# Kernel tuning notes

Measured on AMD Instinct MI355X. Metric: run time of the kernel, lower is better.

Reference implementation:

```python
import jax, jax.numpy as jnp
import numpy as np

K = 9          # neighbors per node (loop=False)
BN_EPS = 1e-5  # BatchNorm2d eps


def setup_inputs() -> dict:
    key = jax.random.key(0)
    k1, k2, k3 = jax.random.split(key, 3)
    B, C, H, W_ = 16, 384, 32, 32
    x = jax.random.normal(k1, (B, C, H, W_), dtype=jnp.float32)
    # GCNConv linear weight (PyG stores [out, in]; y = x @ W.T) and bias
    Wg = jax.random.normal(k2, (C, C), dtype=jnp.float32) / np.sqrt(C)
    bg = jax.random.normal(k3, (C,), dtype=jnp.float32) * 0.02
    gamma = jnp.ones((C,), dtype=jnp.float32)
    beta = jnp.zeros((C,), dtype=jnp.float32)
    return {"x": x, "Wg": Wg, "bg": bg, "gamma": gamma, "beta": beta}


def _knn_indices(xn):
    # xn: [B, N, C] -> neighbor indices [B, N, K] (self excluded)
    sq = jnp.sum(xn * xn, axis=-1)                       # [B, N]
    d = sq[:, :, None] + sq[:, None, :] - 2.0 * jnp.einsum("bnc,bmc->bnm", xn, xn)
    N = xn.shape[1]
    d = d + jnp.eye(N, dtype=xn.dtype) * jnp.finfo(xn.dtype).max  # exclude self
    _, nbr = jax.lax.top_k(-d, K)                        # [B, N, K]
    return nbr


def reference(x, Wg, bg, gamma, beta):
    B, C, H, W_ = x.shape
    N = H * W_
    BN_nodes = B * N
    shortcut = x

    # Flatten to nodes: [B*N, C]
    xn = jnp.transpose(x, (0, 2, 3, 1)).reshape(B, N, C)

    # Per-graph kNN in feature space (PyG knn_graph, flow source_to_target:
    # edges from neighbor (src) to query node (dst))
    nbr = _knn_indices(xn)                                # [B, N, K]
    offs = (jnp.arange(B) * N)[:, None, None]             # [B,1,1]
    src = (nbr + offs).reshape(-1)                        # [B*N*K]
    dst = jnp.broadcast_to(jnp.arange(N)[None, :, None] + offs, (B, N, K)).reshape(-1)

    # GCNConv: add self loops, symmetric normalization
    loops = jnp.arange(BN_nodes)
    src = jnp.concatenate([src, loops])
    dst = jnp.concatenate([dst, loops])

    xw = xn.reshape(BN_nodes, C) @ Wg.T                   # node-wise linear

    deg = jax.ops.segment_sum(jnp.ones_like(dst, dtype=xw.dtype), dst, num_segments=BN_nodes)
    dinv = jax.lax.rsqrt(deg)                             # deg >= 1 due to self loops
    norm = dinv[src] * dinv[dst]                          # [E]

    out = jax.ops.segment_sum(norm[:, None] * xw[src], dst, num_segments=BN_nodes) + bg

    # Back to B x C x H x W
    out = jnp.transpose(out.reshape(B, H, W_, C), (0, 3, 1, 2))

    # BatchNorm2d (training-mode batch statistics, biased variance)
    mu = jnp.mean(out, axis=(0, 2, 3), keepdims=True)
    var = jnp.mean((out - mu) ** 2, axis=(0, 2, 3), keepdims=True)
    out = gamma[None, :, None, None] * (out - mu) * jax.lax.rsqrt(var + BN_EPS) + beta[None, :, None, None]

    # GELU + residual (drop_path = 0 -> identity)
    out = jax.nn.gelu(out) + shortcut
    return out
```

## Files before the change

### kernel.cpp

```cpp
#include <hip/hip_runtime.h>
#include <math.h>

#define B_ 16
#define C_ 384
#define N_ 1024
#define K_ 9

typedef _Float16 f16x8 __attribute__((ext_vector_type(8)));
typedef _Float16 f16x4 __attribute__((ext_vector_type(4)));
typedef float f32x4 __attribute__((ext_vector_type(4)));
typedef unsigned long long u64;

__device__ __forceinline__ void gld_lds16(const void* g, void* l) {
  __builtin_amdgcn_global_load_lds((const __attribute__((address_space(1))) void*)g,
                                   (__attribute__((address_space(3))) void*)l, 16, 0, 0);
}

__global__ void k_cvt(const float* __restrict__ x, ushort* __restrict__ xhT,
                      ushort* __restrict__ xlT) {
  const int bid = blockIdx.x;
  const int ct = bid % 12;
  const int nt = (bid / 12) & 15;
  const int b = bid / 192;
  const int c0 = ct * 32, n0 = nt * 64;
  __shared__ float ld[32 * 65];
  const int t = threadIdx.x;
  {
    const int c = t >> 3, n8 = (t & 7) * 8;
    const float* src = x + ((size_t)(b * C_ + c0 + c) * N_ + n0 + n8);
    float4 v0 = *(const float4*)src;
    float4 v1 = *(const float4*)(src + 4);
    float vv[8] = {v0.x, v0.y, v0.z, v0.w, v1.x, v1.y, v1.z, v1.w};
#pragma unroll
    for (int j = 0; j < 8; ++j) ld[c * 65 + n8 + j] = vv[j];
  }
  __syncthreads();
  {
    const int n = t >> 2, c8 = (t & 3) * 8;
    f16x8 hv, lv;
#pragma unroll
    for (int j = 0; j < 8; ++j) {
      float v = ld[(c8 + j) * 65 + n];
      _Float16 h = (_Float16)v;
      _Float16 l = (_Float16)(v - (float)h);
      hv[j] = h;
      lv[j] = l;
    }
    const size_t off = (size_t)(b * N_ + n0 + n) * C_ + c0 + c8;
    *(f16x8*)(xhT + off) = hv;
    *(f16x8*)(xlT + off) = lv;
  }
}

__global__ void k_cvtw(const float* __restrict__ Wg, ushort* __restrict__ WgH,
                       ushort* __restrict__ WgL) {
  const int i = (blockIdx.x * 256 + threadIdx.x) * 4;
  float4 v = *(const float4*)(Wg + i);
  float vv[4] = {v.x, v.y, v.z, v.w};
  f16x4 hv, lv;
#pragma unroll
  for (int j = 0; j < 4; ++j) {
    _Float16 h = (_Float16)vv[j];
    hv[j] = h;
    lv[j] = (_Float16)(vv[j] - (float)h);
  }
  *(f16x4*)(WgH + i) = hv;
  *(f16x4*)(WgL + i) = lv;
}

__global__ void k_sq(const float* __restrict__ x, float* __restrict__ sq) {
  const int idx = blockIdx.x * blockDim.x + threadIdx.x;
  const int b = idx >> 10, n = idx & 1023;
  const float* xb = x + (size_t)b * C_ * N_ + n;
  double s = 0.0;
#pragma unroll 4
  for (int c = 0; c < C_; ++c) {
    float v = xb[(size_t)c * N_];
    s = fma((double)v, (double)v, s);
  }
  sq[idx] = (float)s;
}

__global__ __launch_bounds__(256, 2) void k_gram(const ushort* __restrict__ xhT,
                                                 const ushort* __restrict__ xlT,
                                                 const float* __restrict__ sq,
                                                 float* __restrict__ D, int base_b, int nb) {
  const int bid = blockIdx.x;
  int b_local, pid;
  if (nb >= 8) {
    const int x = bid & 7, j = bid >> 3, grp = nb >> 3;
    b_local = x * grp + (j >> 6);
    pid = j & 63;
  } else {
    b_local = bid >> 6;
    pid = bid & 63;
  }
  const int b = base_b + b_local;
  const int rt = pid >> 3, mt = pid & 7;
  const int n0 = rt * 128, m0 = mt * 128;

  __shared__ alignas(16) char sm[2][32768];
  const int t = threadIdx.x;
  const int lane = t & 63, wid = t >> 6, quad = lane >> 4, lrow = lane & 15;
  const int wr = wid >> 1, wc = wid & 1;
  const int lrow4 = lane >> 2, lpos = lane & 3;

  const char* src = (const char*)((wid & 1) ? xlT : xhT) +
                    (size_t)(b * N_ + ((wid >> 1) ? m0 : n0)) * C_ * 2;

  f32x4 acc[4][4];
#pragma unroll
  for (int mi = 0; mi < 4; ++mi)
#pragma unroll
    for (int ni = 0; ni < 4; ++ni) acc[mi][ni] = (f32x4){0.f, 0.f, 0.f, 0.f};

  auto stage = [&](int it) {
    char* dst = sm[it & 1] + wid * 8192;
    const int ktB = it * 64;
#pragma unroll
    for (int i = 0; i < 8; ++i) {
      const int row = i * 16 + lrow4;
      const int swz = lpos ^ ((row >> 1) & 3);
      gld_lds16(src + (size_t)row * 768 + ktB + swz * 16, dst + i * 1024 + lane * 16);
    }
  };

  stage(0);
  for (int it = 0; it < 12; ++it) {
    __syncthreads();
    if (it < 11) stage(it + 1);
    const char* smb = sm[it & 1];
    f16x8 ah[4], al[4];
#pragma unroll
    for (int mi = 0; mi < 4; ++mi) {
      const int row = wr * 64 + mi * 16 + lrow;
      const int off = row * 64 + (quad ^ ((row >> 1) & 3)) * 16;
      ah[mi] = *(const f16x8*)(smb + off);
      al[mi] = *(const f16x8*)(smb + 8192 + off);
    }
#pragma unroll
    for (int ni = 0; ni < 4; ++ni) {
      const int row = wc * 64 + ni * 16 + lrow;
      const int off = row * 64 + (quad ^ ((row >> 1) & 3)) * 16;
      f16x8 bh = *(const f16x8*)(smb + 16384 + off);
      f16x8 bl = *(const f16x8*)(smb + 24576 + off);
#pragma unroll
      for (int mi = 0; mi < 4; ++mi) {
        acc[mi][ni] = __builtin_amdgcn_mfma_f32_16x16x32_f16(ah[mi], bh, acc[mi][ni], 0, 0, 0);
        acc[mi][ni] = __builtin_amdgcn_mfma_f32_16x16x32_f16(al[mi], bh, acc[mi][ni], 0, 0, 0);
        acc[mi][ni] = __builtin_amdgcn_mfma_f32_16x16x32_f16(ah[mi], bl, acc[mi][ni], 0, 0, 0);
      }
    }
  }

  const float* sqb = sq + b * N_;
  float sqm[4];
#pragma unroll
  for (int ni = 0; ni < 4; ++ni) sqm[ni] = sqb[m0 + wc * 64 + ni * 16 + lrow];
  float sqn_[4][4];
#pragma unroll
  for (int mi = 0; mi < 4; ++mi)
#pragma unroll
    for (int r = 0; r < 4; ++r) sqn_[mi][r] = sqb[n0 + wr * 64 + mi * 16 + quad * 4 + r];

  float* Db = D + (size_t)b_local * N_ * N_;
#pragma unroll
  for (int mi = 0; mi < 4; ++mi)
#pragma unroll
    for (int ni = 0; ni < 4; ++ni)
#pragma unroll
      for (int r = 0; r < 4; ++r) {
        const int ng = n0 + wr * 64 + mi * 16 + quad * 4 + r;
        const int mg = m0 + wc * 64 + ni * 16 + lrow;
        float d = fmaf(-2.f, acc[mi][ni][r], sqn_[mi][r] + sqm[ni]);
        if (ng == mg) d = 3.402823466e38f;
        Db[(size_t)ng * N_ + mg] = d;
      }
}

__device__ __forceinline__ void ce2f(float& a, float& b) {
  float lo = fminf(a, b), hi = fmaxf(a, b);
  a = lo;
  b = hi;
}

__global__ __launch_bounds__(256) void k_scan(const float* __restrict__ D,
                                              int* __restrict__ nbr, int base_node) {
  const int t = threadIdx.x;
  const int lane = t & 63, wid = t >> 6;
  const int g = lane >> 5;
  const int ll = lane & 31;
  const int nl = blockIdx.x * 8 + wid * 2 + g;
  const float* row = D + (size_t)nl * N_ + ll * 32;
  float v[32];
#pragma unroll
  for (int i = 0; i < 8; ++i) {
    float4 q = *(const float4*)(row + i * 4);
    v[i * 4 + 0] = q.x;
    v[i * 4 + 1] = q.y;
    v[i * 4 + 2] = q.z;
    v[i * 4 + 3] = q.w;
  }
  float key[9];
#pragma unroll
  for (int k = 0; k < 9; ++k) key[k] = 3.402823466e38f;
#pragma unroll
  for (int j = 0; j < 32; ++j) {
    key[8] = fminf(key[8], v[j]);
#pragma unroll
    for (int s = 8; s >= 1; --s) ce2f(key[s - 1], key[s]);
  }
#pragma unroll
  for (int lvl = 1; lvl < 32; lvl <<= 1) {
    float pk[9];
#pragma unroll
    for (int k = 0; k < 9; ++k) pk[k] = __shfl_xor(key[k], lvl, 64);
    float m[9];
#pragma unroll
    for (int k = 0; k < 9; ++k) m[k] = fminf(key[k], pk[8 - k]);
    ce2f(m[0], m[8]);
    ce2f(m[1], m[5]); ce2f(m[2], m[6]); ce2f(m[3], m[7]); ce2f(m[4], m[8]);
    ce2f(m[1], m[3]); ce2f(m[2], m[4]); ce2f(m[5], m[7]); ce2f(m[6], m[8]);
    ce2f(m[1], m[2]); ce2f(m[3], m[4]); ce2f(m[5], m[6]); ce2f(m[7], m[8]);
#pragma unroll
    for (int k = 0; k < 9; ++k) key[k] = m[k];
  }
  const float v9 = key[8];
  int c_lt = 0;
#pragma unroll
  for (int k = 0; k < 8; ++k) c_lt += (key[k] < v9) ? 1 : 0;

  unsigned lt_mask = 0u, eq_mask = 0u;
#pragma unroll
  for (int j = 0; j < 32; ++j) {
    lt_mask |= (v[j] < v9) ? (1u << j) : 0u;
    eq_mask |= (v[j] == v9) ? (1u << j) : 0u;
  }
  const int lt_cnt = __popc(lt_mask), eq_cnt = __popc(eq_mask);
  int packed = lt_cnt | (eq_cnt << 16);
  int run = packed;
#pragma unroll
  for (int off = 1; off < 32; off <<= 1) {
    int q = __shfl_up(run, off, 32);
    if (ll >= off) run += q;
  }
  const int pref = run - packed;
  const int lt_pref = pref & 0xFFFF, eq_pref = pref >> 16;

  int* np = nbr + (size_t)(base_node + nl) * K_;
  int slot = lt_pref;
  unsigned m = lt_mask;
  while (m) {
    int j = __builtin_ctz(m);
    m &= m - 1;
    np[slot++] = ll * 32 + j;
  }
  slot = c_lt + eq_pref;
  m = eq_mask;
  while (m && slot < 9) {
    int j = __builtin_ctz(m);
    m &= m - 1;
    np[slot++] = ll * 32 + j;
  }
}

__global__ __launch_bounds__(256, 3) void k_xw(const ushort* __restrict__ xhT,
                                               const ushort* __restrict__ xlT,
                                               const ushort* __restrict__ WgH,
                                               const ushort* __restrict__ WgL,
                                               float* __restrict__ xw) {
  const int bid = blockIdx.x;
  const int xcd = bid & 7, j = bid >> 3;
  const int pair = xcd * 16 + j / 6;
  const int ct = j % 6;
  const int b = pair >> 3, nt = pair & 7;
  const int co0 = ct * 64, n0 = nt * 128;
  __shared__ alignas(16) char sm[2][24576];
  const int t = threadIdx.x;
  const int lane = t & 63, wid = t >> 6, quad = lane >> 4, lrow = lane & 15;
  const int wr = wid >> 1, wc = wid & 1;
  const int lrow4 = lane >> 2, lpos = lane & 3;

  f32x4 acc[2][4];
#pragma unroll
  for (int mi = 0; mi < 2; ++mi)
#pragma unroll
    for (int ni = 0; ni < 4; ++ni) acc[mi][ni] = (f32x4){0.f, 0.f, 0.f, 0.f};

  const char* asrc[2] = {(const char*)(WgH + (size_t)co0 * C_),
                         (const char*)(WgL + (size_t)co0 * C_)};
  const char* bsrc[2] = {(const char*)(xhT + (size_t)(b * N_ + n0) * C_),
                         (const char*)(xlT + (size_t)(b * N_ + n0) * C_)};

  auto stage = [&](int it) {
    char* dst = sm[it & 1];
    const int ktB = it * 64;
#pragma unroll
    for (int i = 0; i < 6; ++i) {
      const int c = wid * 6 + i;
      const char* src;
      int base, row;
      if (c < 8) {
        const int arr = c >> 2, sub = c & 3;
        src = asrc[arr];
        base = arr * 4096 + sub * 1024;
        row = sub * 16 + lrow4;
      } else {
        const int cc = c - 8, arr = cc >> 3, sub = cc & 7;
        src = bsrc[arr];
        base = 8192 + arr * 8192 + sub * 1024;
        row = sub * 16 + lrow4;
      }
      const int swz = lpos ^ ((row >> 1) & 3);
      gld_lds16(src + (size_t)row * 768 + ktB + swz * 16, dst + base + lane * 16);
    }
  };

  stage(0);
  for (int it = 0; it < 12; ++it) {
    __syncthreads();
    if (it < 11) stage(it + 1);
    const char* smb = sm[it & 1];
    f16x8 bh[4], bl[4];
#pragma unroll
    for (int ni = 0; ni < 4; ++ni) {
      const int row = wr * 64 + ni * 16 + lrow;
      const int off = row * 64 + (quad ^ ((row >> 1) & 3)) * 16;
      bh[ni] = *(const f16x8*)(smb + 8192 + off);
      bl[ni] = *(const f16x8*)(smb + 16384 + off);
    }
#pragma unroll
    for (int mi = 0; mi < 2; ++mi) {
      const int row = wc * 32 + mi * 16 + lrow;
      const int off = row * 64 + (quad ^ ((row >> 1) & 3)) * 16;
      f16x8 ah = *(const f16x8*)(smb + off);
      f16x8 al = *(const f16x8*)(smb + 4096 + off);
#pragma unroll
      for (int ni = 0; ni < 4; ++ni) {
        acc[mi][ni] = __builtin_amdgcn_mfma_f32_16x16x32_f16(ah, bh[ni], acc[mi][ni], 0, 0, 0);
        acc[mi][ni] = __builtin_amdgcn_mfma_f32_16x16x32_f16(al, bh[ni], acc[mi][ni], 0, 0, 0);
        acc[mi][ni] = __builtin_amdgcn_mfma_f32_16x16x32_f16(ah, bl[ni], acc[mi][ni], 0, 0, 0);
      }
    }
  }
#pragma unroll
  for (int mi = 0; mi < 2; ++mi)
#pragma unroll
    for (int ni = 0; ni < 4; ++ni)
#pragma unroll
      for (int r = 0; r < 4; ++r) {
        const int c_g = co0 + wc * 32 + mi * 16 + quad * 4 + r;
        const int n_g = n0 + wr * 64 + ni * 16 + lrow;
        xw[((size_t)b * C_ + c_g) * N_ + n_g] = acc[mi][ni][r];
      }
}

__global__ __launch_bounds__(256) void k_agg(const float* __restrict__ xw,
                                             const int* __restrict__ nbr,
                                             const float* __restrict__ bg,
                                             float* __restrict__ out,
                                             float* __restrict__ stats) {
  const int ct = blockIdx.x % (C_ / 8);
  const int b = blockIdx.x / (C_ / 8);
  const int c0 = ct * 8;
  __shared__ alignas(16) int nb_l[N_ * K_];
  __shared__ alignas(16) float row_l[8][N_ + 4];
  __shared__ float red[2][8][4];
  const int tid = threadIdx.x;
  const int4* gp = (const int4*)(nbr + (size_t)b * N_ * K_);
  int4* lp = (int4*)nb_l;
  for (int t = tid; t < N_ * K_ / 4; t += 256) lp[t] = gp[t];
  for (int t = tid; t < 8 * (N_ / 4); t += 256) {
    const int j = t >> 8, n4 = t & 255;
    float4 v = ((const float4*)(xw + ((size_t)(b * C_ + c0 + j)) * N_))[n4];
    *(float4*)&row_l[j][n4 * 4] = v;
  }
  __syncthreads();
  float bgc[8];
#pragma unroll
  for (int j = 0; j < 8; ++j) bgc[j] = bg[c0 + j];
  float s1[8], s2[8];
#pragma unroll
  for (int j = 0; j < 8; ++j) {
    s1[j] = 0.f;
    s2[j] = 0.f;
  }
  float* outb = out + ((size_t)b * C_ + c0) * N_;
#pragma unroll
  for (int s = 0; s < 4; ++s) {
    const int n = tid + 256 * s;
    const int* nn_ = &nb_l[n * K_];
    int idx[K_];
#pragma unroll
    for (int k = 0; k < K_; ++k) idx[k] = nn_[k];
    float a[8];
#pragma unroll
    for (int j = 0; j < 8; ++j) a[j] = row_l[j][n];
#pragma unroll
    for (int k = 0; k < K_; ++k) {
      const int m = idx[k];
#pragma unroll
      for (int j = 0; j < 8; ++j) a[j] += row_l[j][m];
    }
#pragma unroll
    for (int j = 0; j < 8; ++j) {
      float y = fmaf(a[j], 0.099999994f, bgc[j]);
      outb[(size_t)j * N_ + n] = y;
      s1[j] += y;
      s2[j] = fmaf(y, y, s2[j]);
    }
  }
#pragma unroll
  for (int off = 32; off > 0; off >>= 1)
#pragma unroll
    for (int j = 0; j < 8; ++j) {
      s1[j] += __shfl_down(s1[j], off, 64);
      s2[j] += __shfl_down(s2[j], off, 64);
    }
  const int lane = tid & 63, wid = tid >> 6;
  if (lane == 0)
#pragma unroll
    for (int j = 0; j < 8; ++j) {
      red[0][j][wid] = s1[j];
      red[1][j][wid] = s2[j];
    }
  __syncthreads();
  if (tid < 16) {
    const int j = tid & 7, which = tid >> 3;
    float v = red[which][j][0] + red[which][j][1] + red[which][j][2] + red[which][j][3];
    atomicAdd(&stats[which * C_ + c0 + j], v);
  }
}

__global__ void k_bn(const float* __restrict__ x, const float* __restrict__ gamma,
                     const float* __restrict__ beta, const float* __restrict__ stats,
                     float* __restrict__ out) {
  const int f = blockIdx.x * blockDim.x + threadIdx.x;
  const int e = f * 4;
  const int c = (e >> 10) % C_;
  const float inv = 1.f / 16384.f;
  const float mu = stats[c] * inv;
  const float var = fmaf(-mu, mu, stats[C_ + c] * inv);
  const float sc = gamma[c] * rsqrtf(var + 1e-5f);
  const float sh = fmaf(-mu, sc, beta[c]);
  float4 y = ((const float4*)out)[f];
  float4 xv = ((const float4*)x)[f];
  auto gl = [](float z) {
    float z3 = z * z * z;
    float t = 0.7978845608028654f * fmaf(0.044715f, z3, z);
    float th = tanhf(t);
    return 0.5f * z * (1.f + th);
  };
  float4 o;
  o.x = gl(fmaf(y.x, sc, sh)) + xv.x;
  o.y = gl(fmaf(y.y, sc, sh)) + xv.y;
  o.z = gl(fmaf(y.z, sc, sh)) + xv.z;
  o.w = gl(fmaf(y.w, sc, sh)) + xv.w;
  ((float4*)out)[f] = o;
}

extern "C" void kernel_launch(void* const* d_in, const int* in_sizes, int n_in,
                              void* d_out, int out_size, void* d_ws, size_t ws_size,
                              hipStream_t stream) {
  const float* x = (const float*)d_in[0];
  const float* Wg = (const float*)d_in[1];
  const float* bg = (const float*)d_in[2];
  const float* gamma = (const float*)d_in[3];
  const float* beta = (const float*)d_in[4];
  float* out = (float*)d_out;

  int nb;
  if (ws_size >= 94000000) nb = 16;
  else if (ws_size >= 60500000) nb = 8;
  else nb = 4;

  char* ws = (char*)d_ws;
  ushort* xhT = (ushort*)ws;
  ushort* xlT = (ushort*)(ws + 12582912);
  ushort* WgH = (ushort*)(ws + 25165824);
  ushort* WgL = (ushort*)(ws + 25460736);
  float* sq = (float*)(ws + 25755648);
  float* Dbuf = (float*)(ws + 25821184);
  float* xw = (float*)(ws + 25821184);
  size_t dreg = (size_t)nb * 4194304;
  if (dreg < 25165824) dreg = 25165824;
  int* nbr = (int*)(ws + 25821184 + dreg);
  float* stats = (float*)(ws + 25821184 + dreg + 589824);

  hipMemsetAsync(stats, 0, 2 * C_ * sizeof(float), stream);
  k_cvt<<<3072, 256, 0, stream>>>(x, xhT, xlT);
  k_cvtw<<<144, 256, 0, stream>>>(Wg, WgH, WgL);
  k_sq<<<64, 256, 0, stream>>>(x, sq);
  for (int r = 0; r < B_ / nb; ++r) {
    k_gram<<<nb * 64, 256, 0, stream>>>(xhT, xlT, sq, Dbuf, r * nb, nb);
    k_scan<<<nb * 128, 256, 0, stream>>>(Dbuf, nbr, r * nb * N_);
  }
  k_xw<<<768, 256, 0, stream>>>(xhT, xlT, WgH, WgL, xw);
  k_agg<<<B_ * (C_ / 8), 256, 0, stream>>>(xw, nbr, bg, out, stats);
  k_bn<<<6144, 256, 0, stream>>>(x, gamma, beta, stats, out);
}
```

Before: 244.2 us.

## Exploit Gram matrix symmetry: compute upper-triangle tiles and mirror-store results

The distance-matrix kernel now computes only the 36 upper-triangular 128x128 tiles per graph instead of all 64, and writes each off-diagonal tile's transpose as float4 stores to fill the lower half. To make room for higher occupancy, the low-part operands are loaded directly from global into registers and double-buffered there, which halves LDS use. The launch bound rises to 3 blocks per CU. The intent is to cut MFMA work and input traffic by roughly 44%. In exchange the transposed stores are strided, and register pressure from the prefetched low parts grows.

```diff
diff --git a/kernel.cpp b/kernel.cpp
--- a/kernel.cpp
+++ b/kernel.cpp
@@ -81,32 +81,39 @@
   sq[idx] = (float)s;
 }
 
-__global__ __launch_bounds__(256, 2) void k_gram(const ushort* __restrict__ xhT,
+__global__ __launch_bounds__(256, 3) void k_gram(const ushort* __restrict__ xhT,
                                                  const ushort* __restrict__ xlT,
                                                  const float* __restrict__ sq,
                                                  float* __restrict__ D, int base_b, int nb) {
   const int bid = blockIdx.x;
   int b_local, pid;
   if (nb >= 8) {
-    const int x = bid & 7, j = bid >> 3, grp = nb >> 3;
-    b_local = x * grp + (j >> 6);
-    pid = j & 63;
+    const int xcd = bid & 7, j = bid >> 3, grp = nb >> 3;
+    b_local = xcd * grp + j / 36;
+    pid = j % 36;
   } else {
-    b_local = bid >> 6;
-    pid = bid & 63;
+    b_local = bid / 36;
+    pid = bid % 36;
   }
   const int b = base_b + b_local;
-  const int rt = pid >> 3, mt = pid & 7;
+  int rt = 0, off = 0;
+  while (pid >= off + (8 - rt)) {
+    off += 8 - rt;
+    ++rt;
+  }
+  const int mt = rt + (pid - off);
   const int n0 = rt * 128, m0 = mt * 128;
 
-  __shared__ alignas(16) char sm[2][32768];
+  __shared__ alignas(16) char sm[2][16384];
   const int t = threadIdx.x;
   const int lane = t & 63, wid = t >> 6, quad = lane >> 4, lrow = lane & 15;
   const int wr = wid >> 1, wc = wid & 1;
   const int lrow4 = lane >> 2, lpos = lane & 3;
 
-  const char* src = (const char*)((wid & 1) ? xlT : xhT) +
-                    (size_t)(b * N_ + ((wid >> 1) ? m0 : n0)) * C_ * 2;
+  const char* ah_src = (const char*)xhT + (size_t)(b * N_ + n0) * 768;
+  const char* bh_src = (const char*)xhT + (size_t)(b * N_ + m0) * 768;
+  const char* al_src = (const char*)xlT + (size_t)(b * N_ + n0) * 768;
+  const char* bl_src = (const char*)xlT + (size_t)(b * N_ + m0) * 768;
 
   f32x4 acc[4][4];
 #pragma unroll
@@ -114,41 +121,65 @@
 #pragma unroll
     for (int ni = 0; ni < 4; ++ni) acc[mi][ni] = (f32x4){0.f, 0.f, 0.f, 0.f};
 
+  const int arr = wid >> 1, half = wid & 1;
+  const char* st_src = arr ? bh_src : ah_src;
   auto stage = [&](int it) {
-    char* dst = sm[it & 1] + wid * 8192;
+    char* dst = sm[it & 1] + arr * 8192 + half * 4096;
     const int ktB = it * 64;
 #pragma unroll
-    for (int i = 0; i < 8; ++i) {
-      const int row = i * 16 + lrow4;
+    for (int i = 0; i < 4; ++i) {
+      const int row = half * 64 + i * 16 + lrow4;
       const int swz = lpos ^ ((row >> 1) & 3);
-      gld_lds16(src + (size_t)row * 768 + ktB + swz * 16, dst + i * 1024 + lane * 16);
+      gld_lds16(st_src + (size_t)row * 768 + ktB + swz * 16, dst + i * 1024 + lane * 16);
     }
   };
 
+  f16x8 alc[4], blc[4], aln[4], bln[4];
+  auto load_l = [&](int it, f16x8* a, f16x8* bl_) {
+    const int ktB = it * 64;
+#pragma unroll
+    for (int mi = 0; mi < 4; ++mi) {
+      const int row = wr * 64 + mi * 16 + lrow;
+      a[mi] = *(const f16x8*)(al_src + (size_t)row * 768 + ktB + quad * 16);
+    }
+#pragma unroll
+    for (int ni = 0; ni < 4; ++ni) {
+      const int row = wc * 64 + ni * 16 + lrow;
+      bl_[ni] = *(const f16x8*)(bl_src + (size_t)row * 768 + ktB + quad * 16);
+    }
+  };
+
   stage(0);
+  load_l(0, alc, blc);
   for (int it = 0; it < 12; ++it) {
     __syncthreads();
-    if (it < 11) stage(it + 1);
+    if (it < 11) {
+      stage(it + 1);
+      load_l(it + 1, aln, bln);
+    }
     const char* smb = sm[it & 1];
-    f16x8 ah[4], al[4];
+    f16x8 ah[4];
 #pragma unroll
     for (int mi = 0; mi < 4; ++mi) {
       const int row = wr * 64 + mi * 16 + lrow;
-      const int off = row * 64 + (quad ^ ((row >> 1) & 3)) * 16;
-      ah[mi] = *(const f16x8*)(smb + off);
-      al[mi] = *(const f16x8*)(smb + 8192 + off);
+      ah[mi] = *(const f16x8*)(smb + row * 64 + (quad ^ ((row >> 1) & 3)) * 16);
     }
 #pragma unroll
     for (int ni = 0; ni < 4; ++ni) {
       const int row = wc * 64 + ni * 16 + lrow;
-      const int off = row * 64 + (quad ^ ((row >> 1) & 3)) * 16;
-      f16x8 bh = *(const f16x8*)(smb + 16384 + off);
-      f16x8 bl = *(const f16x8*)(smb + 24576 + off);
+      f16x8 bh = *(const f16x8*)(smb + 8192 + row * 64 + (quad ^ ((row >> 1) & 3)) * 16);
 #pragma unroll
       for (int mi = 0; mi < 4; ++mi) {
         acc[mi][ni] = __builtin_amdgcn_mfma_f32_16x16x32_f16(ah[mi], bh, acc[mi][ni], 0, 0, 0);
-        acc[mi][ni] = __builtin_amdgcn_mfma_f32_16x16x32_f16(al[mi], bh, acc[mi][ni], 0, 0, 0);
-        acc[mi][ni] = __builtin_amdgcn_mfma_f32_16x16x32_f16(ah[mi], bl, acc[mi][ni], 0, 0, 0);
+        acc[mi][ni] = __builtin_amdgcn_mfma_f32_16x16x32_f16(alc[mi], bh, acc[mi][ni], 0, 0, 0);
+        acc[mi][ni] = __builtin_amdgcn_mfma_f32_16x16x32_f16(ah[mi], blc[ni], acc[mi][ni], 0, 0, 0);
+      }
+    }
+    if (it < 11) {
+#pragma unroll
+      for (int i = 0; i < 4; ++i) {
+        alc[i] = aln[i];
+        blc[i] = bln[i];
       }
     }
   }
@@ -164,10 +195,12 @@
     for (int r = 0; r < 4; ++r) sqn_[mi][r] = sqb[n0 + wr * 64 + mi * 16 + quad * 4 + r];
 
   float* Db = D + (size_t)b_local * N_ * N_;
+  const bool mirror = (rt != mt);
 #pragma unroll
   for (int mi = 0; mi < 4; ++mi)
 #pragma unroll
-    for (int ni = 0; ni < 4; ++ni)
+    for (int ni = 0; ni < 4; ++ni) {
+      float dv[4];
 #pragma unroll
       for (int r = 0; r < 4; ++r) {
         const int ng = n0 + wr * 64 + mi * 16 + quad * 4 + r;
@@ -175,7 +208,15 @@
         float d = fmaf(-2.f, acc[mi][ni][r], sqn_[mi][r] + sqm[ni]);
         if (ng == mg) d = 3.402823466e38f;
         Db[(size_t)ng * N_ + mg] = d;
-      }
+        dv[r] = d;
+      }
+      if (mirror) {
+        const int mg = m0 + wc * 64 + ni * 16 + lrow;
+        const int ngb = n0 + wr * 64 + mi * 16 + quad * 4;
+        float4 f4 = {dv[0], dv[1], dv[2], dv[3]};
+        *(float4*)&Db[(size_t)mg * N_ + ngb] = f4;
+      }
+    }
 }
 
 __device__ __forceinline__ void ce2f(float& a, float& b) {
@@ -492,7 +533,7 @@
   k_cvtw<<<144, 256, 0, stream>>>(Wg, WgH, WgL);
   k_sq<<<64, 256, 0, stream>>>(x, sq);
   for (int r = 0; r < B_ / nb; ++r) {
-    k_gram<<<nb * 64, 256, 0, stream>>>(xhT, xlT, sq, Dbuf, r * nb, nb);
+    k_gram<<<nb * 36, 256, 0, stream>>>(xhT, xlT, sq, Dbuf, r * nb, nb);
     k_scan<<<nb * 128, 256, 0, stream>>>(Dbuf, nbr, r * nb * N_);
   }
   k_xw<<<768, 256, 0, stream>>>(xhT, xlT, WgH, WgL, xw);
```

Result: slower. 255.0 us (+4.5%).

## Split squared-norm reduction across channels and single-buffer gram LDS for occupancy

Applied to the files above, without the earlier changes.

The squared-norm kernel, which ran only 64 blocks each looping over all 384 channels, becomes a two-pass reduction. The first pass uses 1024 blocks, each summing 24 channels into double-precision partials. The second pass adds the 16 partials per node. The gram kernel drops its double-buffered LDS staging for a single 32KB buffer with a load-sync-compute-sync pattern, and its launch bounds move from 2 to 4 blocks per SM. This trades prefetch overlap of global loads for higher occupancy, and adds an extra kernel launch plus a partials buffer aliased onto the D region.

```diff
diff --git a/kernel.cpp b/kernel.cpp
--- a/kernel.cpp
+++ b/kernel.cpp
@@ -68,28 +68,39 @@
   *(f16x4*)(WgL + i) = lv;
 }
 
-__global__ void k_sq(const float* __restrict__ x, float* __restrict__ sq) {
+__global__ void k_sq1(const float* __restrict__ x, double* __restrict__ part) {
+  const int bid = blockIdx.x;
+  const int b = bid >> 6, q = (bid >> 2) & 15, nt = bid & 3;
+  const int n = nt * 256 + threadIdx.x;
+  const float* xb = x + ((size_t)b * C_ + q * 24) * N_ + n;
+  double s = 0.0;
+#pragma unroll 4
+  for (int c = 0; c < 24; ++c) {
+    float v = xb[(size_t)c * N_];
+    s = fma((double)v, (double)v, s);
+  }
+  part[((size_t)b * 16 + q) * N_ + n] = s;
+}
+
+__global__ void k_sq2(const double* __restrict__ part, float* __restrict__ sq) {
   const int idx = blockIdx.x * blockDim.x + threadIdx.x;
   const int b = idx >> 10, n = idx & 1023;
-  const float* xb = x + (size_t)b * C_ * N_ + n;
+  const double* p = part + (size_t)b * 16 * N_ + n;
   double s = 0.0;
-#pragma unroll 4
-  for (int c = 0; c < C_; ++c) {
-    float v = xb[(size_t)c * N_];
-    s = fma((double)v, (double)v, s);
-  }
+#pragma unroll
+  for (int q = 0; q < 16; ++q) s += p[(size_t)q * N_];
   sq[idx] = (float)s;
 }
 
-__global__ __launch_bounds__(256, 2) void k_gram(const ushort* __restrict__ xhT,
+__global__ __launch_bounds__(256, 4) void k_gram(const ushort* __restrict__ xhT,
                                                  const ushort* __restrict__ xlT,
                                                  const float* __restrict__ sq,
                                                  float* __restrict__ D, int base_b, int nb) {
   const int bid = blockIdx.x;
   int b_local, pid;
   if (nb >= 8) {
-    const int x = bid & 7, j = bid >> 3, grp = nb >> 3;
-    b_local = x * grp + (j >> 6);
+    const int xcd = bid & 7, j = bid >> 3, grp = nb >> 3;
+    b_local = xcd * grp + (j >> 6);
     pid = j & 63;
   } else {
     b_local = bid >> 6;
@@ -99,7 +110,7 @@
   const int rt = pid >> 3, mt = pid & 7;
   const int n0 = rt * 128, m0 = mt * 128;
 
-  __shared__ alignas(16) char sm[2][32768];
+  __shared__ alignas(16) char sm[32768];
   const int t = threadIdx.x;
   const int lane = t & 63, wid = t >> 6, quad = lane >> 4, lrow = lane & 15;
   const int wr = wid >> 1, wc = wid & 1;
@@ -114,36 +125,32 @@
 #pragma unroll
     for (int ni = 0; ni < 4; ++ni) acc[mi][ni] = (f32x4){0.f, 0.f, 0.f, 0.f};
 
-  auto stage = [&](int it) {
-    char* dst = sm[it & 1] + wid * 8192;
-    const int ktB = it * 64;
-#pragma unroll
-    for (int i = 0; i < 8; ++i) {
-      const int row = i * 16 + lrow4;
-      const int swz = lpos ^ ((row >> 1) & 3);
-      gld_lds16(src + (size_t)row * 768 + ktB + swz * 16, dst + i * 1024 + lane * 16);
-    }
-  };
-
-  stage(0);
   for (int it = 0; it < 12; ++it) {
+    {
+      char* dst = sm + wid * 8192;
+      const int ktB = it * 64;
+#pragma unroll
+      for (int i = 0; i < 8; ++i) {
+        const int row = i * 16 + lrow4;
+        const int swz = lpos ^ ((row >> 1) & 3);
+        gld_lds16(src + (size_t)row * 768 + ktB + swz * 16, dst + i * 1024 + lane * 16);
+      }
+    }
     __syncthreads();
-    if (it < 11) stage(it + 1);
-    const char* smb = sm[it & 1];
     f16x8 ah[4], al[4];
 #pragma unroll
     for (int mi = 0; mi < 4; ++mi) {
       const int row = wr * 64 + mi * 16 + lrow;
       const int off = row * 64 + (quad ^ ((row >> 1) & 3)) * 16;
-      ah[mi] = *(const f16x8*)(smb + off);
-      al[mi] = *(const f16x8*)(smb + 8192 + off);
+      ah[mi] = *(const f16x8*)(sm + off);
+      al[mi] = *(const f16x8*)(sm + 8192 + off);
     }
 #pragma unroll
     for (int ni = 0; ni < 4; ++ni) {
       const int row = wc * 64 + ni * 16 + lrow;
       const int off = row * 64 + (quad ^ ((row >> 1) & 3)) * 16;
-      f16x8 bh = *(const f16x8*)(smb + 16384 + off);
-      f16x8 bl = *(const f16x8*)(smb + 24576 + off);
+      f16x8 bh = *(const f16x8*)(sm + 16384 + off);
+      f16x8 bl = *(const f16x8*)(sm + 24576 + off);
 #pragma unroll
       for (int mi = 0; mi < 4; ++mi) {
         acc[mi][ni] = __builtin_amdgcn_mfma_f32_16x16x32_f16(ah[mi], bh, acc[mi][ni], 0, 0, 0);
@@ -151,6 +158,7 @@
         acc[mi][ni] = __builtin_amdgcn_mfma_f32_16x16x32_f16(ah[mi], bl, acc[mi][ni], 0, 0, 0);
       }
     }
+    if (it < 11) __syncthreads();
   }
 
   const float* sqb = sq + b * N_;
@@ -482,6 +490,7 @@
   float* sq = (float*)(ws + 25755648);
   float* Dbuf = (float*)(ws + 25821184);
   float* xw = (float*)(ws + 25821184);
+  double* sqpart = (double*)(ws + 25821184);
   size_t dreg = (size_t)nb * 4194304;
   if (dreg < 25165824) dreg = 25165824;
   int* nbr = (int*)(ws + 25821184 + dreg);
@@ -490,7 +499,8 @@
   hipMemsetAsync(stats, 0, 2 * C_ * sizeof(float), stream);
   k_cvt<<<3072, 256, 0, stream>>>(x, xhT, xlT);
   k_cvtw<<<144, 256, 0, stream>>>(Wg, WgH, WgL);
-  k_sq<<<64, 256, 0, stream>>>(x, sq);
+  k_sq1<<<1024, 256, 0, stream>>>(x, sqpart);
+  k_sq2<<<64, 256, 0, stream>>>(sqpart, sq);
   for (int r = 0; r < B_ / nb; ++r) {
     k_gram<<<nb * 64, 256, 0, stream>>>(xhT, xlT, sq, Dbuf, r * nb, nb);
     k_scan<<<nb * 128, 256, 0, stream>>>(Dbuf, nbr, r * nb * N_);
```

New measurement: 235.5 us. 1.04x faster.
